# Kernel optimization log

Hardware: AMD Instinct MI355X
Metric: run time of the kernel (lower is better)

## Reference

```python
import jax, jax.numpy as jnp
from jax import lax
import numpy as np

B, N, K = 8, 4096, 64          # clouds, points per cloud, max neighbors
N1, N2 = N // 2, N // 8        # fps ratio 0.5, then 0.25
R1, R2 = 0.2, 0.4              # ball-query radii


def setup_inputs() -> dict:
    key = jax.random.key(0)
    ks = jax.random.split(key, 7)
    def w(k, i, o):
        return jax.random.normal(k, (i, o), jnp.float32) / np.sqrt(i).astype(np.float32)
    return {
        "pos": jax.random.uniform(ks[0], (B, N, 3), jnp.float32),
        "w1a": w(ks[1], 3, 64),    "b1a": jnp.zeros(64, jnp.float32),
        "w1b": w(ks[2], 64, 64),   "b1b": jnp.zeros(64, jnp.float32),
        "w2a": w(ks[3], 67, 128),  "b2a": jnp.zeros(128, jnp.float32),
        "w2b": w(ks[4], 128, 128), "b2b": jnp.zeros(128, jnp.float32),
        "w3a": w(ks[5], 131, 256), "b3a": jnp.zeros(256, jnp.float32),
        "w3b": w(ks[6], 256, 1024),"b3b": jnp.zeros(1024, jnp.float32),
    }


def fps(pos, n_samples):
    # farthest point sampling, deterministic start at index 0. pos: [n, 3]
    d0 = jnp.sum((pos - pos[0]) ** 2, axis=-1)
    def step(mind, _):
        nxt = jnp.argmax(mind)
        d = jnp.sum((pos - pos[nxt]) ** 2, axis=-1)
        return jnp.minimum(mind, d), nxt
    _, idxs = lax.scan(step, d0, None, length=n_samples - 1)
    return jnp.concatenate([jnp.zeros((1,), idxs.dtype), idxs])


def ball_query(centers, pts, r):
    # up to K neighbors within radius r (nearest-first); centers are a subset of pts
    d2 = jnp.sum((centers[:, None, :] - pts[None, :, :]) ** 2, axis=-1)  # [M, n]
    neg = jnp.where(d2 <= r * r, -d2, -jnp.inf)
    vals, nbr = lax.top_k(neg, K)
    return nbr, vals > -jnp.inf  # [M, K] indices, validity mask


def mlp(x, w1, b1, w2, b2, relu_last):
    h = jax.nn.relu(x @ w1 + b1) @ w2 + b2
    return jax.nn.relu(h) if relu_last else h


def masked_max(h, mask):
    # max over neighbor axis; every center has itself as a valid neighbor
    return jnp.max(jnp.where(mask[..., None], h, -jnp.inf), axis=1)


def reference(pos, w1a, b1a, w1b, b1b, w2a, b2a, w2b, b2b, w3a, b3a, w3b, b3b):
    def single(p):  # p: [N, 3]
        # SA1: x is None -> per-edge input is relative position only
        idx1 = fps(p, N1)
        c1 = p[idx1]                                   # [N1, 3]
        nbr1, m1 = ball_query(c1, p, R1)               # [N1, K]
        rel1 = p[nbr1] - c1[:, None, :]                # [N1, K, 3]
        x1 = masked_max(mlp(rel1, w1a, b1a, w1b, b1b, True), m1)   # [N1, 64]
        # SA2: per-edge input is [x_j, pos_j - pos_i]
        idx2 = fps(c1, N2)
        c2 = c1[idx2]                                  # [N2, 3]
        nbr2, m2 = ball_query(c2, c1, R2)              # [N2, K]
        feat2 = jnp.concatenate([x1[nbr2], c1[nbr2] - c2[:, None, :]], axis=-1)  # [N2,K,67]
        x2 = masked_max(mlp(feat2, w2a, b2a, w2b, b2b, True), m2)  # [N2, 128]
        # Global SA: MLP on [x, pos] then global max pool
        g = mlp(jnp.concatenate([x2, c2], axis=-1), w3a, b3a, w3b, b3b, False)   # [N2,1024]
        return jnp.max(g, axis=0)                      # [1024]
    return jax.vmap(single)(pos)                       # [B, 1024]
```

## Files before the change

kernel.cpp:

```cpp
#include <hip/hip_runtime.h>
#include <cstdint>
#include <cstddef>


static constexpr int Bc = 8;
static constexpr int Np = 4096;
static constexpr int Kn = 64;
static constexpr int M1 = 2048;
static constexpr int M2 = 512;
static constexpr int LDX = 132;

#define DEVINL __device__ __forceinline__

DEVINL float d2_exact(float ax, float ay, float az, float bx, float by, float bz) {
    float dx = __fsub_rn(ax, bx);
    float dy = __fsub_rn(ay, by);
    float dz = __fsub_rn(az, bz);
    float xx = __fmul_rn(dx, dx);
    float yy = __fmul_rn(dy, dy);
    float zz = __fmul_rn(dz, dz);
    return __fadd_rn(__fadd_rn(xx, yy), zz);
}

template <int CTRL, int RM, int BM>
DEVINL unsigned long long dpp_max_step(unsigned long long k) {
    unsigned lo = (unsigned)k, hi = (unsigned)(k >> 32);
    unsigned slo = (unsigned)__builtin_amdgcn_update_dpp(0, (int)lo, CTRL, RM, BM, true);
    unsigned shi = (unsigned)__builtin_amdgcn_update_dpp(0, (int)hi, CTRL, RM, BM, true);
    unsigned long long s = ((unsigned long long)shi << 32) | (unsigned long long)slo;
    return s > k ? s : k;
}

DEVINL unsigned long long wave_max_u64_dpp(unsigned long long k) {
    k = dpp_max_step<0x111, 0xf, 0xf>(k);
    k = dpp_max_step<0x112, 0xf, 0xf>(k);
    k = dpp_max_step<0x114, 0xf, 0xf>(k);
    k = dpp_max_step<0x118, 0xf, 0xf>(k);
    k = dpp_max_step<0x142, 0xa, 0xf>(k);
    k = dpp_max_step<0x143, 0xc, 0xf>(k);
    return k;
}

DEVINL unsigned mort3(unsigned v) {
    return (v & 1u) | ((v & 2u) << 2) | ((v & 4u) << 4);
}

DEVINL unsigned cell_of(float x, float y, float z) {
    int ix = (int)(x * 8.0f); ix = ix < 0 ? 0 : (ix > 7 ? 7 : ix);
    int iy = (int)(y * 8.0f); iy = iy < 0 ? 0 : (iy > 7 ? 7 : iy);
    int iz = (int)(z * 8.0f); iz = iz < 0 ? 0 : (iz > 7 ? 7 : iz);
    return mort3((unsigned)ix) | (mort3((unsigned)iy) << 1) | (mort3((unsigned)iz) << 2);
}

DEVINL unsigned* scan512(unsigned* h0, unsigned* h1, int t) {
    unsigned* src = h0; unsigned* dst = h1;
    for (int d = 1; d < 512; d <<= 1) {
        unsigned v = src[t];
        if (t >= d) v += src[t - d];
        dst[t] = v;
        __syncthreads();
        unsigned* tmp = src; src = dst; dst = tmp;
    }
    return src;
}

DEVINL unsigned* scan512x256(unsigned* h0, unsigned* h1, int t) {
    unsigned* src = h0; unsigned* dst = h1;
    for (int d = 1; d < 512; d <<= 1) {
        unsigned a = src[t];
        unsigned b = src[t + 256];
        if (t >= d) a += src[t - d];
        b += src[t + 256 - d];
        dst[t] = a; dst[t + 256] = b;
        __syncthreads();
        unsigned* tmp = src; src = dst; dst = tmp;
    }
    return src;
}

__global__ __launch_bounds__(512)
void fps1_prep_kernel(const float* __restrict__ pos, float* __restrict__ c1,
                      const float* __restrict__ w1a, const float* __restrict__ b1a,
                      const float* __restrict__ w1b, const float* __restrict__ w2a,
                      const float* __restrict__ b2a, const float* __restrict__ w2b,
                      float* __restrict__ w1aT, float* __restrict__ w1bT,
                      float* __restrict__ w2aT, float* __restrict__ w2bT) {
    __shared__ float4 scp[Np];
    __shared__ float s2c[M1 * 3];
    __shared__ unsigned h0[512], h1[512];
    __shared__ unsigned long long slots[3];
    const int t = threadIdx.x;

    if (blockIdx.x >= Bc) {
        int i = (int)(blockIdx.x - Bc) * 512 + t;
        if (i < 64 * 4) {
            int h = i >> 2, d = i & 3;
            w1aT[i] = (d < 3) ? w1a[d * 64 + h] : b1a[h];
        }
        if (i < 64 * 64) {
            int c = i >> 6, h = i & 63;
            w1bT[i] = w1b[h * 64 + c];
        }
        if (i < 128 * 80) {
            int h = i / 80, d = i - h * 80;
            w2aT[i] = (d < 67) ? w2a[d * 128 + h] : ((d == 67) ? b2a[h] : 0.0f);
        }
        {
            int c = i >> 7, h = i & 127;
            w2bT[i] = w2b[h * 128 + c];
        }
        return;
    }

    const int b = blockIdx.x;
    const int lane = t & 63;
    constexpr int NT = 512;
    constexpr int PT = Np / NT;

    const float* base = pos + (size_t)b * Np * 3;
    float gx[PT], gy[PT], gz[PT];
    unsigned gc[PT];
    #pragma unroll
    for (int j = 0; j < PT; ++j) {
        int p = j * NT + t;
        gx[j] = base[p * 3 + 0];
        gy[j] = base[p * 3 + 1];
        gz[j] = base[p * 3 + 2];
        gc[j] = cell_of(gx[j], gy[j], gz[j]);
    }
    float x0 = base[0], y0 = base[1], z0 = base[2];
    h0[t] = 0;
    if (t == 0) { slots[0] = 0; slots[1] = 0; slots[2] = 0; }
    __syncthreads();
    #pragma unroll
    for (int j = 0; j < PT; ++j) atomicAdd(&h0[gc[j]], 1u);
    __syncthreads();
    unsigned cnt = h0[t];
    unsigned* inc = scan512(h0, h1, t);
    inc[t] -= cnt;
    __syncthreads();
    #pragma unroll
    for (int j = 0; j < PT; ++j) {
        unsigned p = atomicAdd(&inc[gc[j]], 1u);
        unsigned key = ((0xFFFu - (unsigned)(j * NT + t)) << 12) | p;
        scp[p] = make_float4(gx[j], gy[j], gz[j], __uint_as_float(key));
    }
    __syncthreads();

    float px[PT], py[PT], pz[PT], mind[PT];
    unsigned oi[PT];
    #pragma unroll
    for (int j = 0; j < PT; ++j) {
        float4 v = scp[t * PT + j];
        px[j] = v.x; py[j] = v.y; pz[j] = v.z;
        oi[j] = __float_as_uint(v.w);
    }
    float lox = px[0], hix = px[0], loy = py[0], hiy = py[0], loz = pz[0], hiz = pz[0];
    #pragma unroll
    for (int j = 1; j < PT; ++j) {
        lox = fminf(lox, px[j]); hix = fmaxf(hix, px[j]);
        loy = fminf(loy, py[j]); hiy = fmaxf(hiy, py[j]);
        loz = fminf(loz, pz[j]); hiz = fmaxf(hiz, pz[j]);
    }

    unsigned long long ck = 0;
    #pragma unroll
    for (int j = 0; j < PT; ++j) {
        float d = d2_exact(px[j], py[j], pz[j], x0, y0, z0);
        mind[j] = d;
        unsigned long long kj =
            ((unsigned long long)__float_as_uint(d) << 24) | (unsigned long long)oi[j];
        if (kj > ck) ck = kj;
    }
    float bmax = __uint_as_float((unsigned)(ck >> 24));
    unsigned long long wkey = wave_max_u64_dpp(ck);
    if (lane == 63) atomicMax(&slots[1], wkey);
    if (t == 0) {
        s2c[0] = x0; s2c[1] = y0; s2c[2] = z0;
    }
    int rd = 1, wr = 2, rs = 0;
    for (int s = 1; s < M1; ++s) {
        __syncthreads();
        unsigned long long km = slots[rd];
        if (t == 0) slots[rs] = 0;
        unsigned spos = (unsigned)km & 0xFFFu;
        float4 cc = scp[spos];
        float cx = cc.x, cy = cc.y, cz = cc.z;
        if (t == 0) {
            s2c[s * 3 + 0] = cx; s2c[s * 3 + 1] = cy; s2c[s * 3 + 2] = cz;
        }
        float dxv = fmaxf(fmaxf(lox - cx, cx - hix), 0.0f);
        float dyv = fmaxf(fmaxf(loy - cy, cy - hiy), 0.0f);
        float dzv = fmaxf(fmaxf(loz - cz, cz - hiz), 0.0f);
        float L = dxv * dxv + dyv * dyv + dzv * dzv;
        bool fire = (L * 0.999f <= bmax);
        if (fire) {
            unsigned long long nck = 0;
            #pragma unroll
            for (int j = 0; j < PT; ++j) {
                float d = d2_exact(px[j], py[j], pz[j], cx, cy, cz);
                float m = fminf(mind[j], d);
                mind[j] = m;
                unsigned long long kj =
                    ((unsigned long long)__float_as_uint(m) << 24) | (unsigned long long)oi[j];
                if (kj > nck) nck = kj;
            }
            ck = nck;
            bmax = __uint_as_float((unsigned)(ck >> 24));
        }
        if (__ballot(fire) != 0ull) wkey = wave_max_u64_dpp(ck);
        if (lane == 63) atomicMax(&slots[wr], wkey);
        int nrd = wr; wr = rs; rs = rd; rd = nrd;
    }
    __syncthreads();
    for (int i = t; i < M1 * 3; i += 512)
        c1[(size_t)b * M1 * 3 + i] = s2c[i];
}

template <int NPT>
DEVINL void bq_body(const float* __restrict__ pts, const float* __restrict__ ctr,
                    int mshift, float r2, int* __restrict__ nbr,
                    uint2* __restrict__ buf, int w, int lane) {
    constexpr int CH = NPT / 64;
    constexpr int CAP = 1024;
    const int b = w >> mshift;
    const float* pb = pts + (size_t)b * NPT * 3;
    const float* cp = ctr + (size_t)w * 3;
    float cx = cp[0], cy = cp[1], cz = cp[2];
    const unsigned r2b = __float_as_uint(r2);

    unsigned ub[CH];
    int cnt = 0;
    #pragma unroll
    for (int j = 0; j < CH; ++j) {
        int p = j * 64 + lane;
        float d = d2_exact(pb[p * 3 + 0], pb[p * 3 + 1], pb[p * 3 + 2], cx, cy, cz);
        ub[j] = __float_as_uint(d);
        cnt += __popcll(__ballot(ub[j] <= r2b));
    }
    int* out = nbr + (size_t)w * Kn;
    const unsigned long long lml = (1ull << lane) - 1ull;

    if (cnt <= Kn) {
        int basep = 0;
        #pragma unroll
        for (int j = 0; j < CH; ++j) {
            bool v = ub[j] <= r2b;
            unsigned long long mk = __ballot(v);
            if (v) out[basep + __popcll(mk & lml)] = j * 64 + lane;
            basep += __popcll(mk);
        }
        if (lane >= cnt) out[lane] = -1;
    } else if (cnt <= CAP) {
        int basep = 0;
        #pragma unroll
        for (int j = 0; j < CH; ++j) {
            bool v = ub[j] <= r2b;
            unsigned long long mk = __ballot(v);
            if (v) buf[basep + __popcll(mk & lml)] =
                       make_uint2(ub[j], (unsigned)(j * 64 + lane));
            basep += __popcll(mk);
        }
        const int C2 = (cnt + 63) >> 6;
        unsigned cb[CAP / 64], ci[CAP / 64];
        #pragma unroll
        for (int e = 0; e < CAP / 64; ++e) {
            if (e >= C2) break;
            int p = e * 64 + lane;
            uint2 v = buf[p];
            cb[e] = (p < cnt) ? v.x : 0xFFFFFFFFu;
            ci[e] = v.y;
        }
        unsigned lo = 0, hi = r2b;
        while (lo < hi) {
            unsigned mid = lo + ((hi - lo) >> 1);
            int c = 0;
            #pragma unroll
            for (int e = 0; e < CAP / 64; ++e) {
                if (e >= C2) break;
                c += __popcll(__ballot(cb[e] <= mid));
            }
            if (c >= Kn) hi = mid; else lo = mid + 1;
        }
        const unsigned tt = lo;
        int cntLess = 0;
        #pragma unroll
        for (int e = 0; e < CAP / 64; ++e) {
            if (e >= C2) break;
            cntLess += __popcll(__ballot(cb[e] < tt));
        }
        const int quota = Kn - cntLess;
        int baseLt = 0, eqseen = 0;
        #pragma unroll
        for (int e = 0; e < CAP / 64; ++e) {
            if (e >= C2) break;
            bool lt = cb[e] < tt;
            bool eq = cb[e] == tt;
            unsigned long long mlt = __ballot(lt);
            unsigned long long meq = __ballot(eq);
            if (lt) out[baseLt + __popcll(mlt & lml)] = (int)ci[e];
            if (eq) {
                int rr = eqseen + __popcll(meq & lml);
                if (rr < quota) out[cntLess + rr] = (int)ci[e];
            }
            baseLt += __popcll(mlt);
            eqseen += __popcll(meq);
        }
    } else {
        unsigned lo = 0, hi = r2b;
        while (lo < hi) {
            unsigned mid = lo + ((hi - lo) >> 1);
            int c = 0;
            #pragma unroll
            for (int j = 0; j < CH; ++j) c += __popcll(__ballot(ub[j] <= mid));
            if (c >= Kn) hi = mid; else lo = mid + 1;
        }
        const unsigned tt = lo;
        int cntLess = 0;
        #pragma unroll
        for (int j = 0; j < CH; ++j) cntLess += __popcll(__ballot(ub[j] < tt));
        const int quota = Kn - cntLess;
        int baseLt = 0, eqseen = 0;
        #pragma unroll
        for (int j = 0; j < CH; ++j) {
            bool lt = ub[j] < tt;
            bool eq = ub[j] == tt;
            unsigned long long mlt = __ballot(lt);
            unsigned long long meq = __ballot(eq);
            if (lt) out[baseLt + __popcll(mlt & lml)] = j * 64 + lane;
            if (eq) {
                int rr = eqseen + __popcll(meq & lml);
                if (rr < quota) out[cntLess + rr] = j * 64 + lane;
            }
            baseLt += __popcll(mlt);
            eqseen += __popcll(meq);
        }
    }
}

static constexpr int K2_LDS = 43040;

__global__ __launch_bounds__(256)
void fps2_bq1_kernel(const float* __restrict__ pos, const float* __restrict__ c1,
                     float* __restrict__ c2, float* __restrict__ X,
                     int* __restrict__ nbr1) {
    extern __shared__ char smem[];
    const int t = threadIdx.x;
    const int lane = t & 63;

    if (blockIdx.x >= Bc) {
        uint2* buf = (uint2*)smem + (size_t)(t >> 6) * 1024;
        int w = __builtin_amdgcn_readfirstlane(
            (int)(blockIdx.x - Bc) * 4 + (t >> 6));
        bq_body<Np>(pos, c1, 11, (float)(0.2 * 0.2), nbr1, buf, w, lane);
        return;
    }

    float4* scp2 = (float4*)smem;
    float* c2buf = (float*)(smem + 32768);
    unsigned* h0 = (unsigned*)(smem + 38912);
    unsigned* h1 = (unsigned*)(smem + 40960);
    unsigned long long* slots = (unsigned long long*)(smem + 43008);

    const int b = blockIdx.x;
    constexpr int NT = 256;
    constexpr int PT = M1 / NT;
    const float* base = c1 + (size_t)b * M1 * 3;

    float gx[PT], gy[PT], gz[PT];
    unsigned gc[PT];
    #pragma unroll
    for (int j = 0; j < PT; ++j) {
        int p = j * NT + t;
        gx[j] = base[p * 3 + 0];
        gy[j] = base[p * 3 + 1];
        gz[j] = base[p * 3 + 2];
        gc[j] = cell_of(gx[j], gy[j], gz[j]);
    }
    float x0 = base[0], y0 = base[1], z0 = base[2];
    h0[t] = 0; h0[t + 256] = 0;
    if (t == 0) { slots[0] = 0; slots[1] = 0; slots[2] = 0; }
    __syncthreads();
    #pragma unroll
    for (int j = 0; j < PT; ++j) atomicAdd(&h0[gc[j]], 1u);
    __syncthreads();
    unsigned cnt0 = h0[t], cnt1 = h0[t + 256];
    unsigned* inc = scan512x256(h0, h1, t);
    inc[t] -= cnt0; inc[t + 256] -= cnt1;
    __syncthreads();
    #pragma unroll
    for (int j = 0; j < PT; ++j) {
        unsigned p = atomicAdd(&inc[gc[j]], 1u);
        unsigned key = ((0xFFFu - (unsigned)(j * NT + t)) << 12) | p;
        scp2[p] = make_float4(gx[j], gy[j], gz[j], __uint_as_float(key));
    }
    __syncthreads();

    float px[PT], py[PT], pz[PT], mind[PT];
    unsigned oi[PT];
    #pragma unroll
    for (int j = 0; j < PT; ++j) {
        float4 v = scp2[t * PT + j];
        px[j] = v.x; py[j] = v.y; pz[j] = v.z;
        oi[j] = __float_as_uint(v.w);
    }
    float lox = px[0], hix = px[0], loy = py[0], hiy = py[0], loz = pz[0], hiz = pz[0];
    #pragma unroll
    for (int j = 1; j < PT; ++j) {
        lox = fminf(lox, px[j]); hix = fmaxf(hix, px[j]);
        loy = fminf(loy, py[j]); hiy = fmaxf(hiy, py[j]);
        loz = fminf(loz, pz[j]); hiz = fmaxf(hiz, pz[j]);
    }

    unsigned long long ck = 0;
    #pragma unroll
    for (int j = 0; j < PT; ++j) {
        float d = d2_exact(px[j], py[j], pz[j], x0, y0, z0);
        mind[j] = d;
        unsigned long long kj =
            ((unsigned long long)__float_as_uint(d) << 24) | (unsigned long long)oi[j];
        if (kj > ck) ck = kj;
    }
    float bmax = __uint_as_float((unsigned)(ck >> 24));
    unsigned long long wkey = wave_max_u64_dpp(ck);
    if (lane == 63) atomicMax(&slots[1], wkey);
    if (t == 0) {
        c2buf[0] = x0; c2buf[1] = y0; c2buf[2] = z0;
    }
    int rd = 1, wr = 2, rs = 0;
    for (int s = 1; s < M2; ++s) {
        __syncthreads();
        unsigned long long km = slots[rd];
        if (t == 0) slots[rs] = 0;
        unsigned spos = (unsigned)km & 0xFFFu;
        float4 cc = scp2[spos];
        float cx = cc.x, cy = cc.y, cz = cc.z;
        if (t == 0) {
            c2buf[s * 3 + 0] = cx; c2buf[s * 3 + 1] = cy; c2buf[s * 3 + 2] = cz;
        }
        float dxv = fmaxf(fmaxf(lox - cx, cx - hix), 0.0f);
        float dyv = fmaxf(fmaxf(loy - cy, cy - hiy), 0.0f);
        float dzv = fmaxf(fmaxf(loz - cz, cz - hiz), 0.0f);
        float L = dxv * dxv + dyv * dyv + dzv * dzv;
        bool fire = (L * 0.999f <= bmax);
        if (fire) {
            unsigned long long nck = 0;
            #pragma unroll
            for (int j = 0; j < PT; ++j) {
                float d = d2_exact(px[j], py[j], pz[j], cx, cy, cz);
                float m = fminf(mind[j], d);
                mind[j] = m;
                unsigned long long kj =
                    ((unsigned long long)__float_as_uint(m) << 24) | (unsigned long long)oi[j];
                if (kj > nck) nck = kj;
            }
            ck = nck;
            bmax = __uint_as_float((unsigned)(ck >> 24));
        }
        if (__ballot(fire) != 0ull) wkey = wave_max_u64_dpp(ck);
        if (lane == 63) atomicMax(&slots[wr], wkey);
        int nrd = wr; wr = rs; rs = rd; rd = nrd;
    }
    __syncthreads();
    for (int i = t; i < M2 * 3; i += 256)
        c2[(size_t)b * M2 * 3 + i] = c2buf[i];
    for (int i = t; i < M2 * 3; i += 256) {
        int s = i / 3, k = i - s * 3;
        X[(size_t)(b * M2 + s) * LDX + 128 + k] = c2buf[i];
    }
}

__global__ __launch_bounds__(256)
void bq2_mlp1_kernel(const float* __restrict__ pos, const float* __restrict__ c1,
                     const float* __restrict__ c2, int* __restrict__ nbr2,
                     const int* __restrict__ nbr1, const float* __restrict__ w1aT,
                     const float* __restrict__ w1bT, const float* __restrict__ b1b,
                     float* __restrict__ x1) {
    __shared__ uint2 cbuf[4][1024];
    const int t = threadIdx.x;
    const int lane = t & 63;
    constexpr int NBQ2 = Bc * M2 / 4;

    if (blockIdx.x < NBQ2) {
        int w = __builtin_amdgcn_readfirstlane((int)blockIdx.x * 4 + (t >> 6));
        bq_body<M1>(c1, c2, 9, (float)(0.4 * 0.4), nbr2, cbuf[t >> 6], w, lane);
        return;
    }

    int w = __builtin_amdgcn_readfirstlane(
        (int)(blockIdx.x - NBQ2) * 4 + (t >> 6));
    const int b = w >> 11;
    const int ii = nbr1[(size_t)w * Kn + lane];
    const bool valid = ii >= 0;
    const int i2 = valid ? ii : 0;
    const float* pp = pos + ((size_t)b * Np + i2) * 3;
    const float* cc = c1 + (size_t)w * 3;
    float rx = pp[0] - cc[0], ry = pp[1] - cc[1], rz = pp[2] - cc[2];
    float h1[64];
    #pragma unroll
    for (int h = 0; h < 64; ++h) {
        float4 wv = ((const float4*)w1aT)[h];
        float a = fmaf(rx, wv.x, fmaf(ry, wv.y, fmaf(rz, wv.z, wv.w)));
        h1[h] = fmaxf(a, 0.0f);
    }
    float* orow = x1 + (size_t)w * 64;
    for (int c4 = 0; c4 < 16; ++c4) {
        float v4[4];
        #pragma unroll
        for (int cq = 0; cq < 4; ++cq) {
            int c = c4 * 4 + cq;
            float acc = b1b[c];
            const float4* wr = (const float4*)(w1bT + (size_t)c * 64);
            #pragma unroll
            for (int q = 0; q < 16; ++q) {
                float4 wv = wr[q];
                acc = fmaf(h1[4 * q + 0], wv.x, acc);
                acc = fmaf(h1[4 * q + 1], wv.y, acc);
                acc = fmaf(h1[4 * q + 2], wv.z, acc);
                acc = fmaf(h1[4 * q + 3], wv.w, acc);
            }
            float v = fmaxf(acc, 0.0f);
            v = valid ? v : -__builtin_inff();
            #pragma unroll
            for (int o = 32; o > 0; o >>= 1) v = fmaxf(v, __shfl_xor(v, o, 64));
            v4[cq] = v;
        }
        if (lane == 0)
            ((float4*)orow)[c4] = make_float4(v4[0], v4[1], v4[2], v4[3]);
    }
}

__global__ __launch_bounds__(256)
void mlp2_kernel(const float* __restrict__ x1, const float* __restrict__ c1,
                 const float* __restrict__ c2, const int* __restrict__ nbr2,
                 const float* __restrict__ w2aT, const float* __restrict__ w2bT,
                 const float* __restrict__ b2b, float* __restrict__ X) {
    const int lane = threadIdx.x & 63;
    int w = __builtin_amdgcn_readfirstlane((int)(blockIdx.x * 4 + (threadIdx.x >> 6)));
    const int b = w >> 9;
    const int ii = nbr2[(size_t)w * Kn + lane];
    const bool valid = ii >= 0;
    const int i2 = valid ? ii : 0;

    float x[68];
    const float4* xr = (const float4*)(x1 + ((size_t)b * M1 + i2) * 64);
    #pragma unroll
    for (int q = 0; q < 16; ++q) {
        float4 v = xr[q];
        x[4 * q + 0] = v.x; x[4 * q + 1] = v.y;
        x[4 * q + 2] = v.z; x[4 * q + 3] = v.w;
    }
    const float* cc = c2 + (size_t)w * 3;
    const float* cp = c1 + ((size_t)b * M1 + i2) * 3;
    x[64] = cp[0] - cc[0];
    x[65] = cp[1] - cc[1];
    x[66] = cp[2] - cc[2];
    x[67] = 0.0f;

    float h1[128];
    #pragma unroll
    for (int h = 0; h < 128; ++h) {
        const float4* r4 = (const float4*)(w2aT + (size_t)h * 80);
        float acc = 0.0f;
        #pragma unroll
        for (int q = 0; q < 16; ++q) {
            float4 wv = r4[q];
            acc = fmaf(x[4 * q + 0], wv.x, acc);
            acc = fmaf(x[4 * q + 1], wv.y, acc);
            acc = fmaf(x[4 * q + 2], wv.z, acc);
            acc = fmaf(x[4 * q + 3], wv.w, acc);
        }
        float4 tl = r4[16];
        acc = fmaf(x[64], tl.x, acc);
        acc = fmaf(x[65], tl.y, acc);
        acc = fmaf(x[66], tl.z, acc);
        acc += tl.w;
        h1[h] = fmaxf(acc, 0.0f);
    }
    float* orow = X + (size_t)w * LDX;
    for (int c4 = 0; c4 < 32; ++c4) {
        float v4[4];
        #pragma unroll
        for (int cq = 0; cq < 4; ++cq) {
            int c = c4 * 4 + cq;
            float acc = b2b[c];
            const float4* wr = (const float4*)(w2bT + (size_t)c * 128);
            #pragma unroll
            for (int q = 0; q < 32; ++q) {
                float4 wv = wr[q];
                acc = fmaf(h1[4 * q + 0], wv.x, acc);
                acc = fmaf(h1[4 * q + 1], wv.y, acc);
                acc = fmaf(h1[4 * q + 2], wv.z, acc);
                acc = fmaf(h1[4 * q + 3], wv.w, acc);
            }
            float v = fmaxf(acc, 0.0f);
            v = valid ? v : -__builtin_inff();
            #pragma unroll
            for (int o = 32; o > 0; o >>= 1) v = fmaxf(v, __shfl_xor(v, o, 64));
            v4[cq] = v;
        }
        if (lane == 0) {
            orow[c4 * 4 + 0] = v4[0]; orow[c4 * 4 + 1] = v4[1];
            orow[c4 * 4 + 2] = v4[2]; orow[c4 * 4 + 3] = v4[3];
        }
    }
}

__global__ __launch_bounds__(256)
void gemm1_kernel(const float* __restrict__ X, const float* __restrict__ w3a,
                  const float* __restrict__ b3a, float* __restrict__ H) {
    const int r = blockIdx.x;
    const int c = threadIdx.x;
    const float* xr = X + (size_t)r * LDX;
    float acc = b3a[c];
    for (int i = 0; i < 131; ++i)
        acc = fmaf(xr[i], w3a[(size_t)i * 256 + c], acc);
    H[(size_t)r * 256 + c] = fmaxf(acc, 0.0f);
}

__global__ __launch_bounds__(256)
void gemm2_kernel(const float* __restrict__ H, const float* __restrict__ w3b,
                  float* __restrict__ part) {
    __shared__ float As[32][33];
    __shared__ float Bs[32][64];
    __shared__ float red[8][64];
    const int bidx = blockIdx.x;
    const int nt = bidx & 15;
    const int mt = (bidx >> 4) & 15;
    const int b = bidx >> 8;
    const int row0 = b * M2 + mt * 32;
    const int col0 = nt * 64;
    const int t = threadIdx.x;
    const int rg = t >> 5, cg = t & 31;

    float acc[4][2] = {{0.f, 0.f}, {0.f, 0.f}, {0.f, 0.f}, {0.f, 0.f}};
    for (int k0 = 0; k0 < 256; k0 += 32) {
        #pragma unroll
        for (int q = 0; q < 4; ++q) {
            int id = t + q * 256;
            As[id >> 5][id & 31] = H[(size_t)(row0 + (id >> 5)) * 256 + k0 + (id & 31)];
        }
        #pragma unroll
        for (int q = 0; q < 8; ++q) {
            int id = t + q * 256;
            Bs[id >> 6][id & 63] = w3b[(size_t)(k0 + (id >> 6)) * 1024 + col0 + (id & 63)];
        }
        __syncthreads();
        #pragma unroll
        for (int kk = 0; kk < 32; ++kk) {
            float b0 = Bs[kk][cg * 2 + 0];
            float b1 = Bs[kk][cg * 2 + 1];
            #pragma unroll
            for (int j = 0; j < 4; ++j) {
                float a = As[rg * 4 + j][kk];
                acc[j][0] = fmaf(a, b0, acc[j][0]);
                acc[j][1] = fmaf(a, b1, acc[j][1]);
            }
        }
        __syncthreads();
    }
    float m0 = fmaxf(fmaxf(acc[0][0], acc[1][0]), fmaxf(acc[2][0], acc[3][0]));
    float m1 = fmaxf(fmaxf(acc[0][1], acc[1][1]), fmaxf(acc[2][1], acc[3][1]));
    red[rg][cg * 2 + 0] = m0;
    red[rg][cg * 2 + 1] = m1;
    __syncthreads();
    if (t < 64) {
        float v = red[0][t];
        #pragma unroll
        for (int q = 1; q < 8; ++q) v = fmaxf(v, red[q][t]);
        part[((size_t)b * 16 + mt) * 1024 + col0 + t] = v;
    }
}

__global__ __launch_bounds__(256)
void rmax_kernel(const float* __restrict__ part, const float* __restrict__ b3b,
                 float* __restrict__ out) {
    int i = blockIdx.x * 256 + threadIdx.x;
    int b = i >> 10, c = i & 1023;
    float v = -__builtin_inff();
    #pragma unroll
    for (int tt = 0; tt < 16; ++tt)
        v = fmaxf(v, part[((size_t)b * 16 + tt) * 1024 + c]);
    out[i] = v + b3b[c];
}

extern "C" void kernel_launch(void* const* d_in, const int* in_sizes, int n_in,
                              void* d_out, int out_size, void* d_ws, size_t ws_size,
                              hipStream_t stream) {
    const float* pos = (const float*)d_in[0];
    const float* w1a = (const float*)d_in[1];
    const float* b1a = (const float*)d_in[2];
    const float* w1b = (const float*)d_in[3];
    const float* b1b = (const float*)d_in[4];
    const float* w2a = (const float*)d_in[5];
    const float* b2a = (const float*)d_in[6];
    const float* w2b = (const float*)d_in[7];
    const float* b2b = (const float*)d_in[8];
    const float* w3a = (const float*)d_in[9];
    const float* b3a = (const float*)d_in[10];
    const float* w3b = (const float*)d_in[11];
    const float* b3b = (const float*)d_in[12];
    float* out = (float*)d_out;

    char* ws = (char*)d_ws;
    size_t off = 0;
    auto alloc = [&](size_t bytes) -> char* {
        char* p = ws + off;
        off += (bytes + 255) & ~(size_t)255;
        return p;
    };
    float* c1   = (float*)alloc(sizeof(float) * Bc * M1 * 3);
    float* c2   = (float*)alloc(sizeof(float) * Bc * M2 * 3);
    int*   nbr1 = (int*)alloc(sizeof(int) * Bc * M1 * Kn);
    int*   nbr2 = (int*)alloc(sizeof(int) * Bc * M2 * Kn);
    float* x1   = (float*)alloc(sizeof(float) * Bc * M1 * 64);
    float* X    = (float*)alloc(sizeof(float) * Bc * M2 * LDX);
    float* H    = (float*)alloc(sizeof(float) * Bc * M2 * 256);
    float* part = (float*)alloc(sizeof(float) * Bc * 16 * 1024);
    float* w1aT = (float*)alloc(sizeof(float) * 64 * 4);
    float* w1bT = (float*)alloc(sizeof(float) * 64 * 64);
    float* w2aT = (float*)alloc(sizeof(float) * 128 * 80);
    float* w2bT = (float*)alloc(sizeof(float) * 128 * 128);

    fps1_prep_kernel<<<dim3(Bc + 32), dim3(512), 0, stream>>>(
        pos, c1, w1a, b1a, w1b, w2a, b2a, w2b, w1aT, w1bT, w2aT, w2bT);
    fps2_bq1_kernel<<<dim3(Bc + Bc * M1 / 4), dim3(256), K2_LDS, stream>>>(
        pos, c1, c2, X, nbr1);
    bq2_mlp1_kernel<<<dim3(Bc * M2 / 4 + Bc * M1 / 4), dim3(256), 0, stream>>>(
        pos, c1, c2, nbr2, nbr1, w1aT, w1bT, b1b, x1);
    mlp2_kernel<<<dim3(Bc * M2 / 4), dim3(256), 0, stream>>>(
        x1, c1, c2, nbr2, w2aT, w2bT, b2b, X);
    gemm1_kernel<<<dim3(Bc * M2), dim3(256), 0, stream>>>(X, w3a, b3a, H);
    gemm2_kernel<<<dim3(Bc * 16 * 16), dim3(256), 0, stream>>>(H, w3b, part);
    rmax_kernel<<<dim3(32), dim3(256), 0, stream>>>(part, b3b, out);
}
```

Baseline: 2.393 ms.

## Recompute ball-query distances instead of caching, split SA2 MLP into two kernels

The ball query no longer keeps all per-lane distances in a register array. Each pass recomputes them from global memory with partial unrolling, which lowers register pressure and so should raise occupancy, at the cost of extra loads and arithmetic. The SA2 MLP is split into a first-layer kernel that writes hidden activations to a workspace buffer and a second-layer kernel that reads them back and does the masked max. The work runs in two batches if the workspace is large enough, trading extra global traffic and launches for fewer live registers per thread.

```diff
diff --git a/kernel.cpp b/kernel.cpp
--- a/kernel.cpp
+++ b/kernel.cpp
@@ -218,47 +218,43 @@
 }
 
 template <int NPT>
-DEVINL void bq_body(const float* __restrict__ pts, const float* __restrict__ ctr,
-                    int mshift, float r2, int* __restrict__ nbr,
-                    uint2* __restrict__ buf, int w, int lane) {
+DEVINL void bq_core(const float* __restrict__ pb, float cx, float cy, float cz,
+                    float r2, int* out, uint2* buf, int lane) {
     constexpr int CH = NPT / 64;
     constexpr int CAP = 1024;
-    const int b = w >> mshift;
-    const float* pb = pts + (size_t)b * NPT * 3;
-    const float* cp = ctr + (size_t)w * 3;
-    float cx = cp[0], cy = cp[1], cz = cp[2];
     const unsigned r2b = __float_as_uint(r2);
-
-    unsigned ub[CH];
+    const unsigned long long lml = (1ull << lane) - 1ull;
+
     int cnt = 0;
-    #pragma unroll
+    #pragma unroll 8
     for (int j = 0; j < CH; ++j) {
         int p = j * 64 + lane;
         float d = d2_exact(pb[p * 3 + 0], pb[p * 3 + 1], pb[p * 3 + 2], cx, cy, cz);
-        ub[j] = __float_as_uint(d);
-        cnt += __popcll(__ballot(ub[j] <= r2b));
-    }
-    int* out = nbr + (size_t)w * Kn;
-    const unsigned long long lml = (1ull << lane) - 1ull;
+        cnt += __popcll(__ballot(__float_as_uint(d) <= r2b));
+    }
 
     if (cnt <= Kn) {
         int basep = 0;
-        #pragma unroll
+        #pragma unroll 8
         for (int j = 0; j < CH; ++j) {
-            bool v = ub[j] <= r2b;
+            int p = j * 64 + lane;
+            float d = d2_exact(pb[p * 3 + 0], pb[p * 3 + 1], pb[p * 3 + 2], cx, cy, cz);
+            bool v = __float_as_uint(d) <= r2b;
             unsigned long long mk = __ballot(v);
-            if (v) out[basep + __popcll(mk & lml)] = j * 64 + lane;
+            if (v) out[basep + __popcll(mk & lml)] = p;
             basep += __popcll(mk);
         }
         if (lane >= cnt) out[lane] = -1;
     } else if (cnt <= CAP) {
         int basep = 0;
-        #pragma unroll
+        #pragma unroll 8
         for (int j = 0; j < CH; ++j) {
-            bool v = ub[j] <= r2b;
+            int p = j * 64 + lane;
+            float d = d2_exact(pb[p * 3 + 0], pb[p * 3 + 1], pb[p * 3 + 2], cx, cy, cz);
+            unsigned ubj = __float_as_uint(d);
+            bool v = ubj <= r2b;
             unsigned long long mk = __ballot(v);
-            if (v) buf[basep + __popcll(mk & lml)] =
-                       make_uint2(ub[j], (unsigned)(j * 64 + lane));
+            if (v) buf[basep + __popcll(mk & lml)] = make_uint2(ubj, (unsigned)p);
             basep += __popcll(mk);
         }
         const int C2 = (cnt + 63) >> 6;
@@ -311,26 +307,34 @@
         while (lo < hi) {
             unsigned mid = lo + ((hi - lo) >> 1);
             int c = 0;
-            #pragma unroll
-            for (int j = 0; j < CH; ++j) c += __popcll(__ballot(ub[j] <= mid));
+            for (int j = 0; j < CH; ++j) {
+                int p = j * 64 + lane;
+                float d = d2_exact(pb[p * 3 + 0], pb[p * 3 + 1], pb[p * 3 + 2], cx, cy, cz);
+                c += __popcll(__ballot(__float_as_uint(d) <= mid));
+            }
             if (c >= Kn) hi = mid; else lo = mid + 1;
         }
         const unsigned tt = lo;
         int cntLess = 0;
-        #pragma unroll
-        for (int j = 0; j < CH; ++j) cntLess += __popcll(__ballot(ub[j] < tt));
+        for (int j = 0; j < CH; ++j) {
+            int p = j * 64 + lane;
+            float d = d2_exact(pb[p * 3 + 0], pb[p * 3 + 1], pb[p * 3 + 2], cx, cy, cz);
+            cntLess += __popcll(__ballot(__float_as_uint(d) < tt));
+        }
         const int quota = Kn - cntLess;
         int baseLt = 0, eqseen = 0;
-        #pragma unroll
         for (int j = 0; j < CH; ++j) {
-            bool lt = ub[j] < tt;
-            bool eq = ub[j] == tt;
+            int p = j * 64 + lane;
+            float d = d2_exact(pb[p * 3 + 0], pb[p * 3 + 1], pb[p * 3 + 2], cx, cy, cz);
+            unsigned ubj = __float_as_uint(d);
+            bool lt = ubj < tt;
+            bool eq = ubj == tt;
             unsigned long long mlt = __ballot(lt);
             unsigned long long meq = __ballot(eq);
-            if (lt) out[baseLt + __popcll(mlt & lml)] = j * 64 + lane;
+            if (lt) out[baseLt + __popcll(mlt & lml)] = p;
             if (eq) {
                 int rr = eqseen + __popcll(meq & lml);
-                if (rr < quota) out[cntLess + rr] = j * 64 + lane;
+                if (rr < quota) out[cntLess + rr] = p;
             }
             baseLt += __popcll(mlt);
             eqseen += __popcll(meq);
@@ -352,7 +356,10 @@
         uint2* buf = (uint2*)smem + (size_t)(t >> 6) * 1024;
         int w = __builtin_amdgcn_readfirstlane(
             (int)(blockIdx.x - Bc) * 4 + (t >> 6));
-        bq_body<Np>(pos, c1, 11, (float)(0.2 * 0.2), nbr1, buf, w, lane);
+        const int b = w >> 11;
+        const float* cr = c1 + (size_t)w * 3;
+        bq_core<Np>(pos + (size_t)b * Np * 3, cr[0], cr[1], cr[2],
+                    (float)(0.2 * 0.2), nbr1 + (size_t)w * Kn, buf, lane);
         return;
     }
 
@@ -483,7 +490,10 @@
 
     if (blockIdx.x < NBQ2) {
         int w = __builtin_amdgcn_readfirstlane((int)blockIdx.x * 4 + (t >> 6));
-        bq_body<M1>(c1, c2, 9, (float)(0.4 * 0.4), nbr2, cbuf[t >> 6], w, lane);
+        const int b = w >> 9;
+        const float* cr = c2 + (size_t)w * 3;
+        bq_core<M1>(c1 + (size_t)b * M1 * 3, cr[0], cr[1], cr[2],
+                    (float)(0.4 * 0.4), nbr2 + (size_t)w * Kn, cbuf[t >> 6], lane);
         return;
     }
 
@@ -527,6 +537,102 @@
         }
         if (lane == 0)
             ((float4*)orow)[c4] = make_float4(v4[0], v4[1], v4[2], v4[3]);
+    }
+}
+
+__global__ __launch_bounds__(256)
+void mlp2a_kernel(const float* __restrict__ x1, const float* __restrict__ c1,
+                  const float* __restrict__ c2, const int* __restrict__ nbr2,
+                  const float* __restrict__ w2aT, float* __restrict__ h1g,
+                  int wbase) {
+    const int lane = threadIdx.x & 63;
+    int wl = __builtin_amdgcn_readfirstlane((int)(blockIdx.x * 4 + (threadIdx.x >> 6)));
+    const int w = wbase + wl;
+    const int b = w >> 9;
+    const int ii = nbr2[(size_t)w * Kn + lane];
+    const bool valid = ii >= 0;
+    const int i2 = valid ? ii : 0;
+
+    float x[68];
+    const float4* xr = (const float4*)(x1 + ((size_t)b * M1 + i2) * 64);
+    #pragma unroll
+    for (int q = 0; q < 16; ++q) {
+        float4 v = xr[q];
+        x[4 * q + 0] = v.x; x[4 * q + 1] = v.y;
+        x[4 * q + 2] = v.z; x[4 * q + 3] = v.w;
+    }
+    const float* cc = c2 + (size_t)w * 3;
+    const float* cp = c1 + ((size_t)b * M1 + i2) * 3;
+    x[64] = cp[0] - cc[0];
+    x[65] = cp[1] - cc[1];
+    x[66] = cp[2] - cc[2];
+    x[67] = 0.0f;
+
+    float* hout = h1g + (size_t)wl * (128 * 64) + lane;
+    #pragma unroll 4
+    for (int h = 0; h < 128; ++h) {
+        const float4* r4 = (const float4*)(w2aT + (size_t)h * 80);
+        float acc = 0.0f;
+        #pragma unroll
+        for (int q = 0; q < 16; ++q) {
+            float4 wv = r4[q];
+            acc = fmaf(x[4 * q + 0], wv.x, acc);
+            acc = fmaf(x[4 * q + 1], wv.y, acc);
+            acc = fmaf(x[4 * q + 2], wv.z, acc);
+            acc = fmaf(x[4 * q + 3], wv.w, acc);
+        }
+        float4 tl = r4[16];
+        acc = fmaf(x[64], tl.x, acc);
+        acc = fmaf(x[65], tl.y, acc);
+        acc = fmaf(x[66], tl.z, acc);
+        acc += tl.w;
+        hout[h * 64] = fmaxf(acc, 0.0f);
+    }
+}
+
+__global__ __launch_bounds__(256)
+void mlp2b_kernel(const float* __restrict__ h1g, const int* __restrict__ nbr2,
+                  const float* __restrict__ w2bT, const float* __restrict__ b2b,
+                  float* __restrict__ X, int wbase) {
+    const int lane = threadIdx.x & 63;
+    int wl = __builtin_amdgcn_readfirstlane((int)(blockIdx.x * 4 + (threadIdx.x >> 6)));
+    const int w = wbase + wl;
+    const int ii = nbr2[(size_t)w * Kn + lane];
+    const bool valid = ii >= 0;
+    const float* hrow = h1g + (size_t)wl * (128 * 64) + lane;
+    float* orow = X + (size_t)w * LDX;
+
+    for (int ct = 0; ct < 16; ++ct) {
+        float acc[8];
+        #pragma unroll
+        for (int o = 0; o < 8; ++o) acc[o] = b2b[ct * 8 + o];
+        for (int q = 0; q < 32; ++q) {
+            float hv0 = hrow[(4 * q + 0) * 64];
+            float hv1 = hrow[(4 * q + 1) * 64];
+            float hv2 = hrow[(4 * q + 2) * 64];
+            float hv3 = hrow[(4 * q + 3) * 64];
+            #pragma unroll
+            for (int o = 0; o < 8; ++o) {
+                int c = ct * 8 + o;
+                float4 wv = ((const float4*)(w2bT + (size_t)c * 128))[q];
+                acc[o] = fmaf(hv0, wv.x, acc[o]);
+                acc[o] = fmaf(hv1, wv.y, acc[o]);
+                acc[o] = fmaf(hv2, wv.z, acc[o]);
+                acc[o] = fmaf(hv3, wv.w, acc[o]);
+            }
+        }
+        #pragma unroll
+        for (int o = 0; o < 8; ++o) {
+            float v = fmaxf(acc[o], 0.0f);
+            v = valid ? v : -__builtin_inff();
+            #pragma unroll
+            for (int os = 32; os > 0; os >>= 1) v = fmaxf(v, __shfl_xor(v, os, 64));
+            acc[o] = v;
+        }
+        if (lane == 0) {
+            #pragma unroll
+            for (int o = 0; o < 8; ++o) orow[ct * 8 + o] = acc[o];
+        }
     }
 }
 
@@ -722,14 +828,31 @@
     float* w2aT = (float*)alloc(sizeof(float) * 128 * 80);
     float* w2bT = (float*)alloc(sizeof(float) * 128 * 128);
 
+    constexpr int NB = 2;
+    constexpr int CPB = Bc * M2 / NB;
+    size_t h1_bytes = (size_t)CPB * 128 * 64 * sizeof(float);
+    bool split_mlp2 = (off + h1_bytes + 256) <= ws_size;
+    float* h1g = split_mlp2 ? (float*)alloc(h1_bytes) : nullptr;
+
     fps1_prep_kernel<<<dim3(Bc + 32), dim3(512), 0, stream>>>(
         pos, c1, w1a, b1a, w1b, w2a, b2a, w2b, w1aT, w1bT, w2aT, w2bT);
     fps2_bq1_kernel<<<dim3(Bc + Bc * M1 / 4), dim3(256), K2_LDS, stream>>>(
         pos, c1, c2, X, nbr1);
     bq2_mlp1_kernel<<<dim3(Bc * M2 / 4 + Bc * M1 / 4), dim3(256), 0, stream>>>(
         pos, c1, c2, nbr2, nbr1, w1aT, w1bT, b1b, x1);
-    mlp2_kernel<<<dim3(Bc * M2 / 4), dim3(256), 0, stream>>>(
-        x1, c1, c2, nbr2, w2aT, w2bT, b2b, X);
+
+    if (split_mlp2) {
+        for (int bt = 0; bt < NB; ++bt) {
+            mlp2a_kernel<<<dim3(CPB / 4), dim3(256), 0, stream>>>(
+                x1, c1, c2, nbr2, w2aT, h1g, bt * CPB);
+            mlp2b_kernel<<<dim3(CPB / 4), dim3(256), 0, stream>>>(
+                h1g, nbr2, w2bT, b2b, X, bt * CPB);
+        }
+    } else {
+        mlp2_kernel<<<dim3(Bc * M2 / 4), dim3(256), 0, stream>>>(
+            x1, c1, c2, nbr2, w2aT, w2bT, b2b, X);
+    }
+
     gemm1_kernel<<<dim3(Bc * M2), dim3(256), 0, stream>>>(X, w3a, b3a, H);
     gemm2_kernel<<<dim3(Bc * 16 * 16), dim3(256), 0, stream>>>(H, w3b, part);
     rmax_kernel<<<dim3(32), dim3(256), 0, stream>>>(part, b3b, out);
```

Result: slower. 2.530 ms (+5.7%).
